# Kernel optimization log

Measured on AMD Instinct MI355X. Metric: run time of the kernel, lower is better.

Reference implementation:

```python
import jax, jax.numpy as jnp
import numpy as np

B, S, D = 1, 2048, 2048        # batch, max_seq_len, hidden_dim_attention
G, HPG = 4, 8                   # n_head_groups, n_heads_per_group
H = G * HPG                     # 32 total heads
DK = D // G                     # 512, KV projection width
HD = D // H                     # 64, head dim
EPS = 1e-6


def _embed_position(x, pm):
    # x: [B, S, d]; pm: [2, 1, S, D] -> uses pm[i][:, :, :d]
    d = x.shape[-1]
    _x = jnp.concatenate([-x[:, :, d // 2:], x[:, :, :d // 2]], axis=-1)
    # Faithful to source: BOTH terms use the rotated _x (source quirk).
    return _x * pm[0][:, :, :d] + _x * pm[1][:, :, :d]


def setup_inputs() -> dict:
    key = jax.random.key(0)
    k0, k1, k2, k3, k4, k5 = jax.random.split(key, 6)
    sc = 1.0 / np.sqrt(D).astype(np.float32)
    x = jax.random.normal(k0, (B, S, D), jnp.float32)
    position_matrix = jax.random.uniform(k1, (2, 1, S, D), jnp.float32)
    Wq = jax.random.normal(k2, (D, D), jnp.float32) * sc
    Wk = jax.random.normal(k3, (DK, D), jnp.float32) * sc
    Wv = jax.random.normal(k4, (DK, D), jnp.float32) * sc
    Wo = jax.random.normal(k5, (D, D), jnp.float32) * sc
    return {"x": x, "position_matrix": position_matrix,
            "Wq": Wq, "Wk": Wk, "Wv": Wv, "Wo": Wo}


def reference(x, position_matrix, Wq, Wk, Wv, Wo):
    xq = x @ Wq.T                                  # [B,S,D]
    xk = x @ Wk.T                                  # [B,S,DK]
    xv = x @ Wv.T                                  # [B,S,DK]
    xq = _embed_position(xq, position_matrix)
    xk = _embed_position(xk, position_matrix)
    # GQA expansion: replicate the DK-wide KV across G groups, split into heads.
    xk4 = jnp.broadcast_to(xk[:, :, None, :], (B, S, G, DK)).reshape(B, S, H, HD).transpose(0, 2, 1, 3)
    xv4 = jnp.broadcast_to(xv[:, :, None, :], (B, S, G, DK)).reshape(B, S, H, HD).transpose(0, 2, 1, 3)
    xq4 = xq.reshape(B, S, H, HD).transpose(0, 2, 1, 3)   # [B,H,S,HD]
    score = jnp.einsum('bhsd,bhtd->bhst', xq4, xk4) / (np.sqrt(DK) + EPS)
    # Source adds a tiny positive value (1e-10) above the diagonal, not -inf.
    mask = jnp.triu(jnp.full((S, S), 1e-10, jnp.float32), 1)
    score = score + mask
    e = jnp.exp(score.astype(jnp.float32))
    scores = (e / (jnp.sum(e, axis=-1, keepdims=True) + 1.0)).astype(xq4.dtype)
    out = jnp.einsum('bhst,bhtd->bhsd', scores, xv4)      # [B,H,S,HD]
    out = out.transpose(0, 2, 1, 3).reshape(B, S, D)
    return out @ Wo.T
```

## Files before the change

kernel.cpp:

```cpp
#include <hip/hip_runtime.h>
#include <cmath>

typedef unsigned short u16;
typedef unsigned int u32;
typedef __bf16 bf16x8 __attribute__((ext_vector_type(8)));
typedef __bf16 bf16x4 __attribute__((ext_vector_type(4)));
typedef float f32x4 __attribute__((ext_vector_type(4)));

#define S_LEN 2048
#define D_MODEL 2048
#define DK_ 512
#define PM1_OFF 4194304
#define CEXP 0.06375872f

__device__ __forceinline__ u16 f2b(float f) {
  u32 u = __float_as_uint(f);
  return (u16)((u + 0x7fffu + ((u >> 16) & 1u)) >> 16);
}

__device__ __forceinline__ void gload_lds16(const void* gp, void* lp) {
  __builtin_amdgcn_global_load_lds(
      (const __attribute__((address_space(1))) void*)gp,
      (__attribute__((address_space(3))) void*)lp, 16, 0, 0);
}

__global__ __launch_bounds__(256) void cast_all_kernel(
    const float* __restrict__ x, const float* __restrict__ wq,
    const float* __restrict__ wk, const float* __restrict__ wv,
    const float* __restrict__ wo,
    u16* __restrict__ xb, u16* __restrict__ wqb, u16* __restrict__ wkb,
    u16* __restrict__ wvb, u16* __restrict__ wob)
{
  long i4 = (long)blockIdx.x * 256 + threadIdx.x;
  const float* src; u16* dst; long off;
  if (i4 < 1048576)       { src = x;  dst = xb;  off = i4; }
  else if (i4 < 2097152)  { src = wq; dst = wqb; off = i4 - 1048576; }
  else if (i4 < 2359296)  { src = wk; dst = wkb; off = i4 - 2097152; }
  else if (i4 < 2621440)  { src = wv; dst = wvb; off = i4 - 2359296; }
  else                    { src = wo; dst = wob; off = i4 - 2621440; }
  float4 v = *(const float4*)(src + off * 4);
  ushort4 o;
  o.x = f2b(v.x); o.y = f2b(v.y); o.z = f2b(v.z); o.w = f2b(v.w);
  *(ushort4*)(dst + off * 4) = o;
}

template<int EPI>
__global__ __launch_bounds__(256) void gemm_bt(
    const u16* __restrict__ A, const u16* __restrict__ B,
    void* __restrict__ C0, void* __restrict__ C1, void* __restrict__ C2,
    int M, int N, int K, const float* __restrict__ pm)
{
  __shared__ u16 As[2][64 * 64];
  __shared__ u16 Bs[2][128 * 64];
  const int tid = threadIdx.x;
  const int lane = tid & 63, w = tid >> 6;
  const int wr = w >> 1, wc = w & 1;
  const int l15 = lane & 15, l4 = lane >> 4;

  const int nwg = gridDim.x * gridDim.y;
  const int orig = blockIdx.y * gridDim.x + blockIdx.x;
  const int lin2 = (orig & 7) * (nwg >> 3) + (orig >> 3);
  const int m0 = (lin2 & 31) * 64;
  const int n0 = (lin2 >> 5) * 128;

  const int srow = tid >> 3;
  const int scol = ((tid & 7) ^ (srow & 7)) << 3;
  const int swz = (l15 & 7) << 3;
  const int ldsoff = (tid >> 6) << 10;
  const u16* gA = A + (size_t)(m0 + srow) * K + scol;
  const u16* gB = B + (size_t)(n0 + srow) * K + scol;

  const f32x4 z4 = {0.f, 0.f, 0.f, 0.f};
  f32x4 acc[2][4];
#pragma unroll
  for (int i = 0; i < 2; ++i)
#pragma unroll
    for (int j = 0; j < 4; ++j) acc[i][j] = z4;

  {
    char* la = (char*)As[0] + ldsoff;
    char* lb = (char*)Bs[0] + ldsoff;
#pragma unroll
    for (int i = 0; i < 2; ++i) gload_lds16(gA + (size_t)(i * 32) * K, la + i * 4096);
#pragma unroll
    for (int i = 0; i < 4; ++i) gload_lds16(gB + (size_t)(i * 32) * K, lb + i * 4096);
  }
  asm volatile("s_waitcnt vmcnt(0)" ::: "memory");
  asm volatile("s_barrier" ::: "memory");

  const int NT = K >> 6;
  int cur = 0;
  for (int t = 0; t < NT; ++t) {
    if (t + 1 < NT) {
      const int kt = (t + 1) << 6;
      char* la = (char*)As[cur ^ 1] + ldsoff;
      char* lb = (char*)Bs[cur ^ 1] + ldsoff;
#pragma unroll
      for (int i = 0; i < 2; ++i) gload_lds16(gA + (size_t)(i * 32) * K + kt, la + i * 4096);
#pragma unroll
      for (int i = 0; i < 4; ++i) gload_lds16(gB + (size_t)(i * 32) * K + kt, lb + i * 4096);
      asm volatile("s_waitcnt vmcnt(6)" ::: "memory");
    } else {
      asm volatile("s_waitcnt vmcnt(0)" ::: "memory");
    }
    asm volatile("s_barrier" ::: "memory");

    const u16* as = As[cur];
    const u16* bs = Bs[cur];
#pragma unroll
    for (int ks = 0; ks < 2; ++ks) {
      bf16x8 a[2], b[4];
#pragma unroll
      for (int mt = 0; mt < 2; ++mt)
        a[mt] = *(const bf16x8*)(&as[(wr * 32 + mt * 16 + l15) * 64 + ((ks * 32 + l4 * 8) ^ swz)]);
#pragma unroll
      for (int nt = 0; nt < 4; ++nt)
        b[nt] = *(const bf16x8*)(&bs[(wc * 64 + nt * 16 + l15) * 64 + ((ks * 32 + l4 * 8) ^ swz)]);
#pragma unroll
      for (int mt = 0; mt < 2; ++mt)
#pragma unroll
        for (int nt = 0; nt < 4; ++nt)
          acc[mt][nt] = __builtin_amdgcn_mfma_f32_16x16x32_bf16(a[mt], b[nt], acc[mt][nt], 0, 0, 0);
    }
    asm volatile("s_barrier" ::: "memory");
    cur ^= 1;
  }

#pragma unroll
  for (int mt = 0; mt < 2; ++mt)
#pragma unroll
    for (int nt = 0; nt < 4; ++nt) {
      const int mb = m0 + wr * 32 + mt * 16 + l4 * 4;
      const int n = n0 + wc * 64 + nt * 16 + l15;
      if (EPI == 2) {
#pragma unroll
        for (int j = 0; j < 4; ++j)
          ((float*)C0)[(size_t)(mb + j) * N + n] = acc[mt][nt][j];
      } else if (n >= 2560) {
        const int c = n - 2560;
        ushort4 q;
        q.x = f2b(acc[mt][nt][0]); q.y = f2b(acc[mt][nt][1]);
        q.z = f2b(acc[mt][nt][2]); q.w = f2b(acc[mt][nt][3]);
        *(ushort4*)((u16*)C2 + (size_t)c * S_LEN + mb) = q;
      } else if (n < 2048) {
        const int jj = (n < 1024) ? (n + 1024) : (n - 1024);
#pragma unroll
        for (int j = 0; j < 4; ++j) {
          const int m = mb + j;
          const float sv = (n < 1024) ? acc[mt][nt][j] : -acc[mt][nt][j];
          const float p = pm[(size_t)m * D_MODEL + jj] +
                          pm[PM1_OFF + (size_t)m * D_MODEL + jj];
          ((u16*)C0)[(size_t)m * D_MODEL + jj] = f2b(sv * p * CEXP);
        }
      } else {
        const int nn = n - 2048;
        const int jj = (nn < 256) ? (nn + 256) : (nn - 256);
#pragma unroll
        for (int j = 0; j < 4; ++j) {
          const int m = mb + j;
          const float sv = (nn < 256) ? acc[mt][nt][j] : -acc[mt][nt][j];
          const float p = pm[(size_t)m * D_MODEL + jj] +
                          pm[PM1_OFF + (size_t)m * D_MODEL + jj];
          ((u16*)C1)[(size_t)m * DK_ + jj] = f2b(sv * p);
        }
      }
    }
}

__global__ __launch_bounds__(256) void attn_kernel(
    const u16* __restrict__ Q, const u16* __restrict__ Kx,
    const u16* __restrict__ Vt, u16* __restrict__ O)
{
  __shared__ u16 Ks[2][64 * 64];
  __shared__ u16 Vs[2][64 * 64];
  __shared__ u16 Es[4 * 32 * 64];

  const int tid = threadIdx.x;
  const int lane = tid & 63, w = tid >> 6;
  const int l15 = lane & 15, l4 = lane >> 4;

  const int orig = blockIdx.y * 16 + blockIdx.x;
  const int lin2 = (orig & 7) * 64 + (orig >> 3);
  const int h = lin2 >> 4;
  const int qb = lin2 & 15;
  const int q0 = qb * 128 + w * 32;
  const int hk = (h & 7) * 64;

  bf16x8 bq[2][2];
#pragma unroll
  for (int g = 0; g < 2; ++g)
#pragma unroll
    for (int ks = 0; ks < 2; ++ks)
      bq[g][ks] = *(const bf16x8*)(Q + (size_t)(q0 + g * 16 + l15) * D_MODEL
                                     + h * 64 + ks * 32 + l4 * 8);

  bf16x8 b1;
#pragma unroll
  for (int i = 0; i < 8; ++i) b1[i] = (__bf16)1.0f;

  const f32x4 z4 = {0.f, 0.f, 0.f, 0.f};
  f32x4 o[2][4], dsum[2];
#pragma unroll
  for (int g = 0; g < 2; ++g) {
    dsum[g] = z4;
#pragma unroll
    for (int nt = 0; nt < 4; ++nt) o[g][nt] = z4;
  }

  u16* Ew = Es + w * (32 * 64);
  const int swz = (l15 & 7) << 3;
  const int srow = tid >> 3;
  const int scol = ((tid & 7) ^ (srow & 7)) << 3;
  const int ldsoff = w << 10;
  const u16* gK = Kx + (size_t)srow * DK_ + hk + scol;
  const u16* gV = Vt + (size_t)(hk + srow) * S_LEN + scol;

  {
    char* lK = (char*)Ks[0] + ldsoff;
    char* lV = (char*)Vs[0] + ldsoff;
    gload_lds16(gK,                        lK);
    gload_lds16(gK + (size_t)32 * DK_,     lK + 4096);
    gload_lds16(gV,                        lV);
    gload_lds16(gV + (size_t)32 * S_LEN,   lV + 4096);
  }
  asm volatile("s_waitcnt vmcnt(0)" ::: "memory");
  asm volatile("s_barrier" ::: "memory");

  int cur = 0;
  for (int t0 = 0; t0 < S_LEN; t0 += 64) {
    if (t0 + 64 < S_LEN) {
      char* lK = (char*)Ks[cur ^ 1] + ldsoff;
      char* lV = (char*)Vs[cur ^ 1] + ldsoff;
      gload_lds16(gK + (size_t)(t0 + 64) * DK_,       lK);
      gload_lds16(gK + (size_t)(t0 + 96) * DK_,       lK + 4096);
      gload_lds16(gV + t0 + 64,                       lV);
      gload_lds16(gV + t0 + 64 + (size_t)32 * S_LEN,  lV + 4096);
      asm volatile("s_waitcnt vmcnt(4)" ::: "memory");
    } else {
      asm volatile("s_waitcnt vmcnt(0)" ::: "memory");
    }
    asm volatile("s_barrier" ::: "memory");

    const u16* ks_ = Ks[cur];
    const u16* vs_ = Vs[cur];

    f32x4 sT[2][4];
#pragma unroll
    for (int g = 0; g < 2; ++g)
#pragma unroll
      for (int tf = 0; tf < 4; ++tf) sT[g][tf] = z4;
#pragma unroll
    for (int ks = 0; ks < 2; ++ks) {
      bf16x8 ak[4];
#pragma unroll
      for (int tf = 0; tf < 4; ++tf)
        ak[tf] = *(const bf16x8*)(&ks_[(tf * 16 + l15) * 64 + ((ks * 32 + l4 * 8) ^ swz)]);
      __builtin_amdgcn_s_setprio(1);
#pragma unroll
      for (int g = 0; g < 2; ++g)
#pragma unroll
        for (int tf = 0; tf < 4; ++tf)
          sT[g][tf] = __builtin_amdgcn_mfma_f32_16x16x32_bf16(ak[tf], bq[g][ks], sT[g][tf], 0, 0, 0);
      __builtin_amdgcn_s_setprio(0);
    }

#pragma unroll
    for (int g = 0; g < 2; ++g)
#pragma unroll
      for (int tf = 0; tf < 4; ++tf) {
        const float e0 = __builtin_amdgcn_exp2f(sT[g][tf][0]);
        const float e1 = __builtin_amdgcn_exp2f(sT[g][tf][1]);
        const float e2 = __builtin_amdgcn_exp2f(sT[g][tf][2]);
        const float e3 = __builtin_amdgcn_exp2f(sT[g][tf][3]);
        bf16x4 pk = {(__bf16)e0, (__bf16)e1, (__bf16)e2, (__bf16)e3};
        *(bf16x4*)(&Ew[(g * 16 + l15) * 64 + ((tf * 16 + l4 * 4) ^ swz)]) = pk;
      }

#pragma unroll
    for (int ks = 0; ks < 2; ++ks) {
      bf16x8 ae[2], bv[4];
#pragma unroll
      for (int g = 0; g < 2; ++g)
        ae[g] = *(const bf16x8*)(&Ew[(g * 16 + l15) * 64 + ((ks * 32 + l4 * 8) ^ swz)]);
#pragma unroll
      for (int nt = 0; nt < 4; ++nt)
        bv[nt] = *(const bf16x8*)(&vs_[(nt * 16 + l15) * 64 + ((ks * 32 + l4 * 8) ^ swz)]);
      __builtin_amdgcn_s_setprio(1);
#pragma unroll
      for (int g = 0; g < 2; ++g) {
#pragma unroll
        for (int nt = 0; nt < 4; ++nt)
          o[g][nt] = __builtin_amdgcn_mfma_f32_16x16x32_bf16(ae[g], bv[nt], o[g][nt], 0, 0, 0);
        dsum[g] = __builtin_amdgcn_mfma_f32_16x16x32_bf16(ae[g], b1, dsum[g], 0, 0, 0);
      }
      __builtin_amdgcn_s_setprio(0);
    }

    asm volatile("s_barrier" ::: "memory");
    cur ^= 1;
  }

#pragma unroll
  for (int g = 0; g < 2; ++g) {
    float dn[4];
#pragma unroll
    for (int j = 0; j < 4; ++j) dn[j] = dsum[g][j] + 1.0f;
#pragma unroll
    for (int nt = 0; nt < 4; ++nt)
#pragma unroll
      for (int j = 0; j < 4; ++j) {
        O[(size_t)(q0 + g * 16 + l4 * 4 + j) * D_MODEL + h * 64 + nt * 16 + l15] =
            f2b(o[g][nt][j] / dn[j]);
      }
  }
}

extern "C" void kernel_launch(void* const* d_in, const int* in_sizes, int n_in,
                              void* d_out, int out_size, void* d_ws, size_t ws_size,
                              hipStream_t stream) {
  const float* x  = (const float*)d_in[0];
  const float* pm = (const float*)d_in[1];
  const float* Wq = (const float*)d_in[2];
  const float* Wk = (const float*)d_in[3];
  const float* Wv = (const float*)d_in[4];
  const float* Wo = (const float*)d_in[5];
  float* outp = (float*)d_out;
  char* ws = (char*)d_ws;

  const size_t MB = 1024 * 1024;
  u16* xb   = (u16*)(ws + 0 * MB);
  u16* wqb  = (u16*)(ws + 8 * MB);
  u16* wkb  = (u16*)(ws + 16 * MB);
  u16* wvb  = (u16*)(ws + 18 * MB);
  u16* wob  = (u16*)(ws + 20 * MB);
  u16* qro  = (u16*)(ws + 28 * MB);
  u16* kro  = (u16*)(ws + 36 * MB);
  u16* xvt  = (u16*)(ws + 40 * MB);
  u16* attn = (u16*)(ws + 42 * MB);
  const u16* wqkv = wqb;

  cast_all_kernel<<<14336, 256, 0, stream>>>(x, Wq, Wk, Wv, Wo, xb, wqb, wkb, wvb, wob);
  gemm_bt<1><<<dim3(24, 32), 256, 0, stream>>>(xb, wqkv, (void*)qro, (void*)kro,
                                               (void*)xvt, 2048, 3072, 2048, pm);
  attn_kernel<<<dim3(16, 32), 256, 0, stream>>>(qro, kro, xvt, attn);
  gemm_bt<2><<<dim3(16, 32), 256, 0, stream>>>(attn, wob, (void*)outp, nullptr,
                                               nullptr, 2048, 2048, 2048, nullptr);
}
```

Before: 133.8 us.

## Triple-buffer K/V tiles and software-pipeline next QK^T ahead of PV

The attention loop moves from double to triple buffering of K/V tiles in LDS, so loads are issued two tiles ahead. The QK^T MFMAs for the next tile are computed before the PV MFMAs of the current tile, which overlaps exp/LDS work with matrix ops across iterations. The cost is more LDS per block, which may lower occupancy, plus more live accumulator registers from carrying sT across iterations.

Result: no change. 135.7 us (+1.4%).

```diff
diff --git a/kernel.cpp b/kernel.cpp
--- a/kernel.cpp
+++ b/kernel.cpp
@@ -171,9 +171,9 @@
     const u16* __restrict__ Q, const u16* __restrict__ Kx,
     const u16* __restrict__ Vt, u16* __restrict__ O)
 {
-  __shared__ u16 Ks[2][64 * 64];
-  __shared__ u16 Vs[2][64 * 64];
-  __shared__ u16 Es[4 * 32 * 64];
+  __shared__ u16 Ks[3][64 * 64];
+  __shared__ u16 Vs[3][64 * 64];
+  __shared__ u16 Es[4][32 * 64];
 
   const int tid = threadIdx.x;
   const int lane = tid & 63, w = tid >> 6;
@@ -199,15 +199,15 @@
   for (int i = 0; i < 8; ++i) b1[i] = (__bf16)1.0f;
 
   const f32x4 z4 = {0.f, 0.f, 0.f, 0.f};
-  f32x4 o[2][4], dsum[2];
+  f32x4 o[2][4], dsum[2], sT[2][4];
 #pragma unroll
   for (int g = 0; g < 2; ++g) {
     dsum[g] = z4;
 #pragma unroll
-    for (int nt = 0; nt < 4; ++nt) o[g][nt] = z4;
-  }
-
-  u16* Ew = Es + w * (32 * 64);
+    for (int nt = 0; nt < 4; ++nt) { o[g][nt] = z4; sT[g][nt] = z4; }
+  }
+
+  u16* Ew = Es[w];
   const int swz = (l15 & 7) << 3;
   const int srow = tid >> 3;
   const int scol = ((tid & 7) ^ (srow & 7)) << 3;
@@ -215,54 +215,44 @@
   const u16* gK = Kx + (size_t)srow * DK_ + hk + scol;
   const u16* gV = Vt + (size_t)(hk + srow) * S_LEN + scol;
 
-  {
-    char* lK = (char*)Ks[0] + ldsoff;
-    char* lV = (char*)Vs[0] + ldsoff;
-    gload_lds16(gK,                        lK);
-    gload_lds16(gK + (size_t)32 * DK_,     lK + 4096);
-    gload_lds16(gV,                        lV);
-    gload_lds16(gV + (size_t)32 * S_LEN,   lV + 4096);
-  }
-  asm volatile("s_waitcnt vmcnt(0)" ::: "memory");
+#define STAGE_KV(b, tt) {                                            \
+    char* lK = (char*)Ks[b] + ldsoff;                                \
+    char* lV = (char*)Vs[b] + ldsoff;                                \
+    gload_lds16(gK + (size_t)((tt) * 64) * DK_,        lK);          \
+    gload_lds16(gK + (size_t)((tt) * 64 + 32) * DK_,   lK + 4096);   \
+    gload_lds16(gV + (tt) * 64,                        lV);          \
+    gload_lds16(gV + (tt) * 64 + (size_t)32 * S_LEN,   lV + 4096); }
+
+#define QK_TILE(ksrc, dst)                                                          \
+for (int ks = 0; ks < 2; ++ks) {                                                    \
+      bf16x8 ak[4];                                                                 \
+      _Pragma("unroll")                                                             \
+      for (int tf = 0; tf < 4; ++tf)                                                \
+        ak[tf] = *(const bf16x8*)(&(ksrc)[(tf * 16 + l15) * 64 +                    \
+                                          ((ks * 32 + l4 * 8) ^ swz)]);             \
+      __builtin_amdgcn_s_setprio(1);                                                \
+      _Pragma("unroll")                                                             \
+      for (int g = 0; g < 2; ++g)                                                   \
+        _Pragma("unroll")                                                           \
+        for (int tf = 0; tf < 4; ++tf)                                              \
+          (dst)[g][tf] = __builtin_amdgcn_mfma_f32_16x16x32_bf16(                   \
+              ak[tf], bq[g][ks], (dst)[g][tf], 0, 0, 0);                            \
+      __builtin_amdgcn_s_setprio(0);                                                \
+    }
+
+  STAGE_KV(0, 0);
+  STAGE_KV(1, 1);
+  asm volatile("s_waitcnt vmcnt(4)" ::: "memory");
   asm volatile("s_barrier" ::: "memory");
-
-  int cur = 0;
-  for (int t0 = 0; t0 < S_LEN; t0 += 64) {
-    if (t0 + 64 < S_LEN) {
-      char* lK = (char*)Ks[cur ^ 1] + ldsoff;
-      char* lV = (char*)Vs[cur ^ 1] + ldsoff;
-      gload_lds16(gK + (size_t)(t0 + 64) * DK_,       lK);
-      gload_lds16(gK + (size_t)(t0 + 96) * DK_,       lK + 4096);
-      gload_lds16(gV + t0 + 64,                       lV);
-      gload_lds16(gV + t0 + 64 + (size_t)32 * S_LEN,  lV + 4096);
-      asm volatile("s_waitcnt vmcnt(4)" ::: "memory");
-    } else {
-      asm volatile("s_waitcnt vmcnt(0)" ::: "memory");
-    }
+  QK_TILE(Ks[0], sT);
+
+  const int NT = 32;
+  for (int t = 0; t < NT; ++t) {
+    const int bc = t % 3;
+    const int bn = (t + 1) % 3;
+    const int bf = (t + 2) % 3;
     asm volatile("s_barrier" ::: "memory");
-
-    const u16* ks_ = Ks[cur];
-    const u16* vs_ = Vs[cur];
-
-    f32x4 sT[2][4];
-#pragma unroll
-    for (int g = 0; g < 2; ++g)
-#pragma unroll
-      for (int tf = 0; tf < 4; ++tf) sT[g][tf] = z4;
-#pragma unroll
-    for (int ks = 0; ks < 2; ++ks) {
-      bf16x8 ak[4];
-#pragma unroll
-      for (int tf = 0; tf < 4; ++tf)
-        ak[tf] = *(const bf16x8*)(&ks_[(tf * 16 + l15) * 64 + ((ks * 32 + l4 * 8) ^ swz)]);
-      __builtin_amdgcn_s_setprio(1);
-#pragma unroll
-      for (int g = 0; g < 2; ++g)
-#pragma unroll
-        for (int tf = 0; tf < 4; ++tf)
-          sT[g][tf] = __builtin_amdgcn_mfma_f32_16x16x32_bf16(ak[tf], bq[g][ks], sT[g][tf], 0, 0, 0);
-      __builtin_amdgcn_s_setprio(0);
-    }
+    if (t + 2 < NT) STAGE_KV(bf, t + 2);
 
 #pragma unroll
     for (int g = 0; g < 2; ++g)
@@ -276,6 +266,19 @@
         *(bf16x4*)(&Ew[(g * 16 + l15) * 64 + ((tf * 16 + l4 * 4) ^ swz)]) = pk;
       }
 
+    if (t + 1 < NT) {
+      if (t + 2 < NT) asm volatile("s_waitcnt vmcnt(4)" ::: "memory");
+      else            asm volatile("s_waitcnt vmcnt(0)" ::: "memory");
+    }
+    asm volatile("s_barrier" ::: "memory");
+
+    f32x4 sTn[2][4];
+#pragma unroll
+    for (int g = 0; g < 2; ++g)
+#pragma unroll
+      for (int tf = 0; tf < 4; ++tf) sTn[g][tf] = z4;
+    if (t + 1 < NT) { QK_TILE(Ks[bn], sTn); }
+
 #pragma unroll
     for (int ks = 0; ks < 2; ++ks) {
       bf16x8 ae[2], bv[4];
@@ -284,7 +287,7 @@
         ae[g] = *(const bf16x8*)(&Ew[(g * 16 + l15) * 64 + ((ks * 32 + l4 * 8) ^ swz)]);
 #pragma unroll
       for (int nt = 0; nt < 4; ++nt)
-        bv[nt] = *(const bf16x8*)(&vs_[(nt * 16 + l15) * 64 + ((ks * 32 + l4 * 8) ^ swz)]);
+        bv[nt] = *(const bf16x8*)(&Vs[bc][(nt * 16 + l15) * 64 + ((ks * 32 + l4 * 8) ^ swz)]);
       __builtin_amdgcn_s_setprio(1);
 #pragma unroll
       for (int g = 0; g < 2; ++g) {
@@ -296,9 +299,13 @@
       __builtin_amdgcn_s_setprio(0);
     }
 
-    asm volatile("s_barrier" ::: "memory");
-    cur ^= 1;
-  }
+#pragma unroll
+    for (int g = 0; g < 2; ++g)
+#pragma unroll
+      for (int tf = 0; tf < 4; ++tf) sT[g][tf] = sTn[g][tf];
+  }
+#undef STAGE_KV
+#undef QK_TILE
 
 #pragma unroll
   for (int g = 0; g < 2; ++g) {
```
